# Kernel tuning notes

Hardware: AMD Instinct MI355X
Metric: run time of the kernel (lower is better)

The kernel has to match this reference:

```python
import jax, jax.numpy as jnp
import numpy as np

BETA = 0.1
TRUNC = 1.0
MIN_VALID_RATIO = 0.3


def _wls_affine(x, y, w):
    # Weighted least squares fit of y ~ s*x + t over the last axis.
    sw = w.sum(-1)
    swx = (w * x).sum(-1)
    swy = (w * y).sum(-1)
    swxx = (w * x * x).sum(-1)
    swxy = (w * x * y).sum(-1)
    det = sw * swxx - swx * swx
    det = jnp.where(jnp.abs(det) < 1e-12, 1e-12, det)
    s = (sw * swxy - swx * swy) / det
    t = (swxx * swy - swx * swxy) / det
    return s, t


def _align_depth_affine(x, y, w, trunc):
    # Truncated robust affine alignment: initial WLS fit, then refit with
    # weights of points whose weighted residual exceeds `trunc` zeroed out
    # (falling back to the original weights if everything is truncated).
    s0, t0 = _wls_affine(x, y, w)
    e = w * jnp.abs(s0[..., None] * x + t0[..., None] - y)
    w2 = w * (e < trunc).astype(w.dtype)
    w2 = jnp.where(w2.sum(-1, keepdims=True) > 1e-8, w2, w)
    return _wls_affine(x, y, w2)


def _smooth(err, beta):
    if beta == 0:
        return err
    return jnp.where(err < beta, 0.5 * err * err / beta, err - 0.5 * beta)


def setup_inputs() -> dict:
    key = jax.random.key(0)
    k1, k2, k3 = jax.random.split(key, 3)
    B = 8
    P = 4096  # num_patches
    K = 256   # patch_pixel_count
    N = P * K
    pred_depth = jax.random.uniform(k1, (B, N), jnp.float32, 0.05, 5.0)
    gt_depth = jax.random.uniform(k2, (B, N), jnp.float32, 0.05, 5.0)
    mask = jax.random.bernoulli(k3, 0.8, (B, N))
    global_scale = jnp.ones((B,), jnp.float32)
    return {
        "pred_depth": pred_depth,
        "gt_depth": gt_depth,
        "mask": mask,
        "global_scale": global_scale,
        "num_patches": P,
        "patch_pixel_count": K,
    }


def reference(pred_depth, gt_depth, mask, global_scale, num_patches, patch_pixel_count):
    B = pred_depth.shape[0]
    P, K = num_patches, patch_pixel_count
    x = pred_depth.reshape(B, P, K)
    y = gt_depth.reshape(B, P, K)
    m = mask.reshape(B, P, K).astype(x.dtype)

    valid_ratio = m.mean(-1)                      # (B, P)
    msum = m.sum(-1)
    mean_depth = jnp.where(msum > 0, (y * m).sum(-1) / jnp.maximum(msum, 1.0), 1.0)

    w = m / jnp.maximum(y, 1e-5)                  # alignment weights (B, P, K)
    s, t = _align_depth_affine(x, y, w, TRUNC)    # (B, P) scale / shift per patch

    ratio = s / jnp.maximum(global_scale[:, None], 1e-12)
    gs_ok = jnp.where(global_scale[:, None] > 0, (ratio >= 0.1) & (ratio <= 10.0), True)
    valid = (valid_ratio >= MIN_VALID_RATIO) & (s > 0) & gs_ok  # (B, P)

    aligned = s[..., None] * x + t[..., None]
    pw = m / jnp.maximum(y, 0.1 * mean_depth[..., None])
    patch_loss = _smooth(jnp.abs(aligned - y) * pw, BETA).mean(-1)  # (B, P)

    vf = valid.astype(x.dtype)
    cnt = vf.sum()
    loss = jnp.where(cnt > 0, (patch_loss * vf).sum() / jnp.maximum(cnt, 1.0), 0.0)
    return loss
```

## Files before the change

kernel.cpp:

```cpp
#include <hip/hip_runtime.h>


#define WPB 4
#define PPW 4
#define NSLOTS 64
#define MAXBLK 2048

__device__ __forceinline__ float wredu(float v) {
#define DPP_ADD(ctrl)                                                        \
  v += __int_as_float(__builtin_amdgcn_update_dpp(                           \
      0, __float_as_int(v), (ctrl), 0xf, 0xf, true))
  DPP_ADD(0x111);
  DPP_ADD(0x112);
  DPP_ADD(0x114);
  DPP_ADD(0x118);
  DPP_ADD(0x142);
  DPP_ADD(0x143);
#undef DPP_ADD
  return __int_as_float(__builtin_amdgcn_readlane(__float_as_int(v), 63));
}

__device__ __forceinline__ float rowredu(float v) {
#define DPP_ADD(ctrl)                                                        \
  v += __int_as_float(__builtin_amdgcn_update_dpp(                           \
      0, __float_as_int(v), (ctrl), 0xf, 0xf, true))
  DPP_ADD(0x121);
  DPP_ADD(0x122);
  DPP_ADD(0x124);
  DPP_ADD(0x128);
#undef DPP_ADD
  return v;
}

__device__ __forceinline__ float frcp(float x) {
  return __builtin_amdgcn_rcpf(x);
}

__global__ __launch_bounds__(256) void moge_patch_kernel(
    const float* __restrict__ xg,
    const float* __restrict__ yg,
    const int*   __restrict__ mg,
    const float* __restrict__ gsg,
    const int*   __restrict__ pP,
    const int*   __restrict__ pK,
    int B,
    float* __restrict__ ws) {
  const int P = pP[0];
  const int K = pK[0];
  const int lane = threadIdx.x & 63;
  const int wib  = threadIdx.x >> 6;
  const int total_patches = B * P;
  const float invK = 1.0f / (float)K;

  float wloss = 0.f, wcnt = 0.f;

  if (K == 256) {
    const int row = lane >> 4;
    const int col = lane & 15;
    const int poff = col * 16;
    const int wave_stride = gridDim.x * WPB * PPW;

    for (int pbase = (blockIdx.x * WPB + wib) * PPW; pbase < total_patches;
         pbase += wave_stride) {
      const int patch = pbase + row;
      const bool row_ok = patch < total_patches;
      const long base = (row_ok ? (long)patch * 256L : 0L) + poff;

      float4 xa[4], ya[4]; int4 ma[4];
      #pragma unroll
      for (int j = 0; j < 4; ++j) {
        xa[j] = *(const float4*)(xg + base + 4 * j);
        ya[j] = *(const float4*)(yg + base + 4 * j);
        ma[j] = *(const int4*)(mg + base + 4 * j);
      }
      const float* xr = (const float*)xa;
      const float* yr = (const float*)ya;
      const int*   mi = (const int*)ma;
      float wv[16];

      float sw = 0.f, swx = 0.f, swy = 0.f, swxx = 0.f, swxy = 0.f;
      float msum = 0.f, symsum = 0.f;
      #pragma unroll
      for (int i = 0; i < 16; ++i) {
        const float m = mi[i] ? 1.f : 0.f;
        const float xx = xr[i], yy = yr[i];
        const float w = m * frcp(fmaxf(yy, 1e-5f));
        wv[i] = w;
        const float wx = w * xx;
        sw += w; swx += wx; swy = fmaf(w, yy, swy);
        swxx = fmaf(wx, xx, swxx); swxy = fmaf(wx, yy, swxy);
        msum += m; symsum = fmaf(m, yy, symsum);
      }
      sw = rowredu(sw); swx = rowredu(swx); swy = rowredu(swy);
      swxx = rowredu(swxx); swxy = rowredu(swxy);

      float det = sw * swxx - swx * swx;
      if (fabsf(det) < 1e-12f) det = 1e-12f;
      float rdet = frcp(det);
      const float s0 = (sw * swxy - swx * swy) * rdet;
      const float t0 = (swxx * swy - swx * swxy) * rdet;

      float sw2 = 0.f, swx2 = 0.f, swy2 = 0.f, swxx2 = 0.f, swxy2 = 0.f;
      #pragma unroll
      for (int i = 0; i < 16; ++i) {
        const float xx = xr[i], yy = yr[i], w = wv[i];
        const float e = w * fabsf(fmaf(s0, xx, t0) - yy);
        const float w2 = (e < 1.0f) ? w : 0.f;
        const float w2x = w2 * xx;
        sw2 += w2; swx2 += w2x; swy2 = fmaf(w2, yy, swy2);
        swxx2 = fmaf(w2x, xx, swxx2); swxy2 = fmaf(w2x, yy, swxy2);
      }
      sw2 = rowredu(sw2); swx2 = rowredu(swx2); swy2 = rowredu(swy2);
      swxx2 = rowredu(swxx2); swxy2 = rowredu(swxy2);
      msum = rowredu(msum); symsum = rowredu(symsum);

      if (sw2 > 1e-8f) {
        sw = sw2; swx = swx2; swy = swy2; swxx = swxx2; swxy = swxy2;
      }
      det = sw * swxx - swx * swx;
      if (fabsf(det) < 1e-12f) det = 1e-12f;
      rdet = frcp(det);
      const float s = (sw * swxy - swx * swy) * rdet;
      const float t = (swxx * swy - swx * swxy) * rdet;

      const float mean_depth =
          (msum > 0.f) ? (symsum * frcp(fmaxf(msum, 1.f))) : 1.f;
      const float yfloor = 0.1f * mean_depth;

      float lsum = 0.f;
      #pragma unroll
      for (int i = 0; i < 16; ++i) {
        const float m = (wv[i] > 0.f) ? 1.f : 0.f;
        const float pw = m * frcp(fmaxf(yr[i], yfloor));
        const float err = fabsf(fmaf(s, xr[i], t) - yr[i]) * pw;
        lsum += (err < 0.1f) ? (5.0f * err * err) : (err - 0.05f);
      }
      const float patch_loss = rowredu(lsum) * invK;

      const int pidx = row_ok ? patch : (total_patches - 1);
      const float gs = gsg[(unsigned)pidx / (unsigned)P];
      const float ratio = s * frcp(fmaxf(gs, 1e-12f));
      const bool gs_ok = (gs > 0.f) ? (ratio >= 0.1f && ratio <= 10.0f) : true;
      const bool valid = (msum * invK >= 0.3f) && (s > 0.f) && gs_ok;

      if (col == 0 && row_ok && valid) { wloss += patch_loss; wcnt += 1.f; }
    }
  } else {
    const int wave_stride = gridDim.x * WPB;
    for (int patch = blockIdx.x * WPB + wib; patch < total_patches;
         patch += wave_stride) {
      const long base = (long)patch * (long)K;
      const float* xp = xg + base;
      const float* yp = yg + base;
      const int*   mp = mg + base;

      float sw = 0.f, swx = 0.f, swy = 0.f, swxx = 0.f, swxy = 0.f;
      float msum = 0.f, symsum = 0.f;
      for (int j = lane; j < K; j += 64) {
        const float m = mp[j] ? 1.f : 0.f;
        const float xx = xp[j], yy = yp[j];
        const float w = m * frcp(fmaxf(yy, 1e-5f));
        const float wx = w * xx;
        sw += w; swx += wx; swy = fmaf(w, yy, swy);
        swxx = fmaf(wx, xx, swxx); swxy = fmaf(wx, yy, swxy);
        msum += m; symsum = fmaf(m, yy, symsum);
      }
      sw = wredu(sw); swx = wredu(swx); swy = wredu(swy);
      swxx = wredu(swxx); swxy = wredu(swxy);
      msum = wredu(msum); symsum = wredu(symsum);

      float det = sw * swxx - swx * swx;
      if (fabsf(det) < 1e-12f) det = 1e-12f;
      float rdet = frcp(det);
      const float s0 = (sw * swxy - swx * swy) * rdet;
      const float t0 = (swxx * swy - swx * swxy) * rdet;

      float sw2 = 0.f, swx2 = 0.f, swy2 = 0.f, swxx2 = 0.f, swxy2 = 0.f;
      for (int j = lane; j < K; j += 64) {
        const float m = mp[j] ? 1.f : 0.f;
        const float xx = xp[j], yy = yp[j];
        const float w = m * frcp(fmaxf(yy, 1e-5f));
        const float e = w * fabsf(fmaf(s0, xx, t0) - yy);
        const float w2 = (e < 1.0f) ? w : 0.f;
        const float w2x = w2 * xx;
        sw2 += w2; swx2 += w2x; swy2 = fmaf(w2, yy, swy2);
        swxx2 = fmaf(w2x, xx, swxx2); swxy2 = fmaf(w2x, yy, swxy2);
      }
      sw2 = wredu(sw2); swx2 = wredu(swx2); swy2 = wredu(swy2);
      swxx2 = wredu(swxx2); swxy2 = wredu(swxy2);

      if (sw2 > 1e-8f) {
        sw = sw2; swx = swx2; swy = swy2; swxx = swxx2; swxy = swxy2;
      }
      det = sw * swxx - swx * swx;
      if (fabsf(det) < 1e-12f) det = 1e-12f;
      rdet = frcp(det);
      const float s = (sw * swxy - swx * swy) * rdet;
      const float t = (swxx * swy - swx * swxy) * rdet;

      const float mean_depth =
          (msum > 0.f) ? (symsum * frcp(fmaxf(msum, 1.f))) : 1.f;
      const float yfloor = 0.1f * mean_depth;

      float lsum = 0.f;
      for (int j = lane; j < K; j += 64) {
        const float m = mp[j] ? 1.f : 0.f;
        const float xx = xp[j], yy = yp[j];
        const float pw = m * frcp(fmaxf(yy, yfloor));
        const float err = fabsf(fmaf(s, xx, t) - yy) * pw;
        lsum += (err < 0.1f) ? (5.0f * err * err) : (err - 0.05f);
      }
      const float patch_loss = wredu(lsum) * invK;

      const float gs = gsg[(unsigned)patch / (unsigned)P];
      const float ratio = s * frcp(fmaxf(gs, 1e-12f));
      const bool gs_ok = (gs > 0.f) ? (ratio >= 0.1f && ratio <= 10.0f) : true;
      const bool valid = (msum * invK >= 0.3f) && (s > 0.f) && gs_ok;

      if (lane == 0 && valid) { wloss += patch_loss; wcnt += 1.f; }
    }
  }

  wloss = wredu(wloss);
  wcnt  = wredu(wcnt);
  __shared__ float sl[WPB], sc[WPB];
  if (lane == 0) { sl[wib] = wloss; sc[wib] = wcnt; }
  __syncthreads();
  if (threadIdx.x == 0) {
    float bl = 0.f, bc = 0.f;
    #pragma unroll
    for (int i = 0; i < WPB; ++i) { bl += sl[i]; bc += sc[i]; }
    const int slot = (blockIdx.x & (NSLOTS - 1)) * 32;
    atomicAdd(&ws[slot], bl);
    atomicAdd(&ws[slot + 1], bc);
  }
}

__global__ void finalize_kernel(const float* __restrict__ ws,
                                float* __restrict__ out) {
  const int t = threadIdx.x;
  float l = wredu(ws[t * 32]);
  float c = wredu(ws[t * 32 + 1]);
  if (t == 0) out[0] = (c > 0.f) ? (l / fmaxf(c, 1.f)) : 0.f;
}

extern "C" void kernel_launch(void* const* d_in, const int* in_sizes, int n_in,
                              void* d_out, int out_size, void* d_ws, size_t ws_size,
                              hipStream_t stream) {
  const float* pred = (const float*)d_in[0];
  const float* gt   = (const float*)d_in[1];
  const int*   mask = (const int*)d_in[2];
  const float* gs   = (const float*)d_in[3];
  const int*   pP   = (const int*)d_in[4];
  const int*   pK   = (const int*)d_in[5];
  const int B = in_sizes[3];
  const long total_pixels = (long)in_sizes[0];
  float* ws = (float*)d_ws;

  hipMemsetAsync(ws, 0, NSLOTS * 32 * sizeof(float), stream);

  long est_patches = total_pixels / 256;
  long blocks = (est_patches + WPB * PPW - 1) / (WPB * PPW);
  if (blocks < 1) blocks = 1;
  if (blocks > MAXBLK) blocks = MAXBLK;
  moge_patch_kernel<<<(int)blocks, 256, 0, stream>>>(pred, gt, mask, gs, pP,
                                                     pK, B, ws);
  finalize_kernel<<<1, 64, 0, stream>>>(ws, (float*)d_out);
}
```

Before: 127.9 us.

## Prefetch next patch group in registers, drop memset and atomics for per-block partials

The K=256 loop is restructured to load the next iteration's x, y and mask vectors into registers before computing the current patch group, giving software double buffering that hides global-memory latency. The grid cap is halved so each wave handles more iterations, and per-block partial sums are written directly to distinct workspace slots instead of atomically added into 64 slots. This lets the hipMemsetAsync launch be removed, and a 256-thread finalize kernel reduces all block partials. The cost is doubled register use for the staged tiles, which may lower occupancy, plus one redundant prefetch on the last iteration.

```diff
diff --git a/kernel.cpp b/kernel.cpp
--- a/kernel.cpp
+++ b/kernel.cpp
@@ -3,8 +3,7 @@
 
 #define WPB 4
 #define PPW 4
-#define NSLOTS 64
-#define MAXBLK 2048
+#define MAXBLK 1024
 
 __device__ __forceinline__ float wredu(float v) {
 #define DPP_ADD(ctrl)                                                        \
@@ -60,90 +59,116 @@
     const int poff = col * 16;
     const int wave_stride = gridDim.x * WPB * PPW;
 
-    for (int pbase = (blockIdx.x * WPB + wib) * PPW; pbase < total_patches;
-         pbase += wave_stride) {
-      const int patch = pbase + row;
-      const bool row_ok = patch < total_patches;
-      const long base = (row_ok ? (long)patch * 256L : 0L) + poff;
-
+    int pbase = (blockIdx.x * WPB + wib) * PPW;
+    if (pbase < total_patches) {
       float4 xa[4], ya[4]; int4 ma[4];
-      #pragma unroll
-      for (int j = 0; j < 4; ++j) {
-        xa[j] = *(const float4*)(xg + base + 4 * j);
-        ya[j] = *(const float4*)(yg + base + 4 * j);
-        ma[j] = *(const int4*)(mg + base + 4 * j);
-      }
-      const float* xr = (const float*)xa;
-      const float* yr = (const float*)ya;
-      const int*   mi = (const int*)ma;
-      float wv[16];
-
-      float sw = 0.f, swx = 0.f, swy = 0.f, swxx = 0.f, swxy = 0.f;
-      float msum = 0.f, symsum = 0.f;
-      #pragma unroll
-      for (int i = 0; i < 16; ++i) {
-        const float m = mi[i] ? 1.f : 0.f;
-        const float xx = xr[i], yy = yr[i];
-        const float w = m * frcp(fmaxf(yy, 1e-5f));
-        wv[i] = w;
-        const float wx = w * xx;
-        sw += w; swx += wx; swy = fmaf(w, yy, swy);
-        swxx = fmaf(wx, xx, swxx); swxy = fmaf(wx, yy, swxy);
-        msum += m; symsum = fmaf(m, yy, symsum);
-      }
-      sw = rowredu(sw); swx = rowredu(swx); swy = rowredu(swy);
-      swxx = rowredu(swxx); swxy = rowredu(swxy);
-
-      float det = sw * swxx - swx * swx;
-      if (fabsf(det) < 1e-12f) det = 1e-12f;
-      float rdet = frcp(det);
-      const float s0 = (sw * swxy - swx * swy) * rdet;
-      const float t0 = (swxx * swy - swx * swxy) * rdet;
-
-      float sw2 = 0.f, swx2 = 0.f, swy2 = 0.f, swxx2 = 0.f, swxy2 = 0.f;
-      #pragma unroll
-      for (int i = 0; i < 16; ++i) {
-        const float xx = xr[i], yy = yr[i], w = wv[i];
-        const float e = w * fabsf(fmaf(s0, xx, t0) - yy);
-        const float w2 = (e < 1.0f) ? w : 0.f;
-        const float w2x = w2 * xx;
-        sw2 += w2; swx2 += w2x; swy2 = fmaf(w2, yy, swy2);
-        swxx2 = fmaf(w2x, xx, swxx2); swxy2 = fmaf(w2x, yy, swxy2);
-      }
-      sw2 = rowredu(sw2); swx2 = rowredu(swx2); swy2 = rowredu(swy2);
-      swxx2 = rowredu(swxx2); swxy2 = rowredu(swxy2);
-      msum = rowredu(msum); symsum = rowredu(symsum);
-
-      if (sw2 > 1e-8f) {
-        sw = sw2; swx = swx2; swy = swy2; swxx = swxx2; swxy = swxy2;
-      }
-      det = sw * swxx - swx * swx;
-      if (fabsf(det) < 1e-12f) det = 1e-12f;
-      rdet = frcp(det);
-      const float s = (sw * swxy - swx * swy) * rdet;
-      const float t = (swxx * swy - swx * swxy) * rdet;
-
-      const float mean_depth =
-          (msum > 0.f) ? (symsum * frcp(fmaxf(msum, 1.f))) : 1.f;
-      const float yfloor = 0.1f * mean_depth;
-
-      float lsum = 0.f;
-      #pragma unroll
-      for (int i = 0; i < 16; ++i) {
-        const float m = (wv[i] > 0.f) ? 1.f : 0.f;
-        const float pw = m * frcp(fmaxf(yr[i], yfloor));
-        const float err = fabsf(fmaf(s, xr[i], t) - yr[i]) * pw;
-        lsum += (err < 0.1f) ? (5.0f * err * err) : (err - 0.05f);
-      }
-      const float patch_loss = rowredu(lsum) * invK;
-
-      const int pidx = row_ok ? patch : (total_patches - 1);
-      const float gs = gsg[(unsigned)pidx / (unsigned)P];
-      const float ratio = s * frcp(fmaxf(gs, 1e-12f));
-      const bool gs_ok = (gs > 0.f) ? (ratio >= 0.1f && ratio <= 10.0f) : true;
-      const bool valid = (msum * invK >= 0.3f) && (s > 0.f) && gs_ok;
-
-      if (col == 0 && row_ok && valid) { wloss += patch_loss; wcnt += 1.f; }
+      {
+        const int patch0 = pbase + row;
+        const long base =
+            ((patch0 < total_patches) ? (long)patch0 * 256L : 0L) + poff;
+        #pragma unroll
+        for (int j = 0; j < 4; ++j) {
+          xa[j] = *(const float4*)(xg + base + 4 * j);
+          ya[j] = *(const float4*)(yg + base + 4 * j);
+          ma[j] = *(const int4*)(mg + base + 4 * j);
+        }
+      }
+
+      for (;;) {
+        const int nbase_p = pbase + wave_stride;
+        const bool has_next = nbase_p < total_patches;
+        float4 nxa[4], nya[4]; int4 nma[4];
+        {
+          const int np = nbase_p + row;
+          const long nb =
+              ((has_next && np < total_patches) ? (long)np * 256L : 0L) + poff;
+          #pragma unroll
+          for (int j = 0; j < 4; ++j) {
+            nxa[j] = *(const float4*)(xg + nb + 4 * j);
+            nya[j] = *(const float4*)(yg + nb + 4 * j);
+            nma[j] = *(const int4*)(mg + nb + 4 * j);
+          }
+        }
+
+        const int patch = pbase + row;
+        const bool row_ok = patch < total_patches;
+        const float* xr = (const float*)xa;
+        const float* yr = (const float*)ya;
+        const int*   mi = (const int*)ma;
+        float wv[16];
+
+        float sw = 0.f, swx = 0.f, swy = 0.f, swxx = 0.f, swxy = 0.f;
+        float msum = 0.f, symsum = 0.f;
+        #pragma unroll
+        for (int i = 0; i < 16; ++i) {
+          const float m = mi[i] ? 1.f : 0.f;
+          const float xx = xr[i], yy = yr[i];
+          const float w = m * frcp(fmaxf(yy, 1e-5f));
+          wv[i] = w;
+          const float wx = w * xx;
+          sw += w; swx += wx; swy = fmaf(w, yy, swy);
+          swxx = fmaf(wx, xx, swxx); swxy = fmaf(wx, yy, swxy);
+          msum += m; symsum = fmaf(m, yy, symsum);
+        }
+        sw = rowredu(sw); swx = rowredu(swx); swy = rowredu(swy);
+        swxx = rowredu(swxx); swxy = rowredu(swxy);
+
+        float det = sw * swxx - swx * swx;
+        if (fabsf(det) < 1e-12f) det = 1e-12f;
+        float rdet = frcp(det);
+        const float s0 = (sw * swxy - swx * swy) * rdet;
+        const float t0 = (swxx * swy - swx * swxy) * rdet;
+
+        float sw2 = 0.f, swx2 = 0.f, swy2 = 0.f, swxx2 = 0.f, swxy2 = 0.f;
+        #pragma unroll
+        for (int i = 0; i < 16; ++i) {
+          const float xx = xr[i], yy = yr[i], w = wv[i];
+          const float e = w * fabsf(fmaf(s0, xx, t0) - yy);
+          const float w2 = (e < 1.0f) ? w : 0.f;
+          const float w2x = w2 * xx;
+          sw2 += w2; swx2 += w2x; swy2 = fmaf(w2, yy, swy2);
+          swxx2 = fmaf(w2x, xx, swxx2); swxy2 = fmaf(w2x, yy, swxy2);
+        }
+        sw2 = rowredu(sw2); swx2 = rowredu(swx2); swy2 = rowredu(swy2);
+        swxx2 = rowredu(swxx2); swxy2 = rowredu(swxy2);
+        msum = rowredu(msum); symsum = rowredu(symsum);
+
+        if (sw2 > 1e-8f) {
+          sw = sw2; swx = swx2; swy = swy2; swxx = swxx2; swxy = swxy2;
+        }
+        det = sw * swxx - swx * swx;
+        if (fabsf(det) < 1e-12f) det = 1e-12f;
+        rdet = frcp(det);
+        const float s = (sw * swxy - swx * swy) * rdet;
+        const float t = (swxx * swy - swx * swxy) * rdet;
+
+        const float mean_depth =
+            (msum > 0.f) ? (symsum * frcp(fmaxf(msum, 1.f))) : 1.f;
+        const float yfloor = 0.1f * mean_depth;
+
+        float lsum = 0.f;
+        #pragma unroll
+        for (int i = 0; i < 16; ++i) {
+          const float m = (wv[i] > 0.f) ? 1.f : 0.f;
+          const float pw = m * frcp(fmaxf(yr[i], yfloor));
+          const float err = fabsf(fmaf(s, xr[i], t) - yr[i]) * pw;
+          lsum += (err < 0.1f) ? (5.0f * err * err) : (err - 0.05f);
+        }
+        const float patch_loss = rowredu(lsum) * invK;
+
+        const int pidx = row_ok ? patch : (total_patches - 1);
+        const float gs = gsg[(unsigned)pidx / (unsigned)P];
+        const float ratio = s * frcp(fmaxf(gs, 1e-12f));
+        const bool gs_ok = (gs > 0.f) ? (ratio >= 0.1f && ratio <= 10.0f) : true;
+        const bool valid = (msum * invK >= 0.3f) && (s > 0.f) && gs_ok;
+
+        if (col == 0 && row_ok && valid) { wloss += patch_loss; wcnt += 1.f; }
+
+        if (!has_next) break;
+        pbase = nbase_p;
+        #pragma unroll
+        for (int j = 0; j < 4; ++j) { xa[j] = nxa[j]; ya[j] = nya[j]; ma[j] = nma[j]; }
+      }
     }
   } else {
     const int wave_stride = gridDim.x * WPB;
@@ -230,18 +255,29 @@
     float bl = 0.f, bc = 0.f;
     #pragma unroll
     for (int i = 0; i < WPB; ++i) { bl += sl[i]; bc += sc[i]; }
-    const int slot = (blockIdx.x & (NSLOTS - 1)) * 32;
-    atomicAdd(&ws[slot], bl);
-    atomicAdd(&ws[slot + 1], bc);
+    ws[blockIdx.x * 32]     = bl;
+    ws[blockIdx.x * 32 + 1] = bc;
   }
 }
 
-__global__ void finalize_kernel(const float* __restrict__ ws,
-                                float* __restrict__ out) {
-  const int t = threadIdx.x;
-  float l = wredu(ws[t * 32]);
-  float c = wredu(ws[t * 32 + 1]);
-  if (t == 0) out[0] = (c > 0.f) ? (l / fmaxf(c, 1.f)) : 0.f;
+__global__ __launch_bounds__(256) void finalize_kernel(
+    const float* __restrict__ ws, float* __restrict__ out, int nblocks) {
+  const int lane = threadIdx.x & 63;
+  const int wib  = threadIdx.x >> 6;
+  float l = 0.f, c = 0.f;
+  for (int i = threadIdx.x; i < nblocks; i += 256) {
+    l += ws[i * 32];
+    c += ws[i * 32 + 1];
+  }
+  l = wredu(l); c = wredu(c);
+  __shared__ float sl[4], sc[4];
+  if (lane == 0) { sl[wib] = l; sc[wib] = c; }
+  __syncthreads();
+  if (threadIdx.x == 0) {
+    const float L = sl[0] + sl[1] + sl[2] + sl[3];
+    const float C = sc[0] + sc[1] + sc[2] + sc[3];
+    out[0] = (C > 0.f) ? (L / fmaxf(C, 1.f)) : 0.f;
+  }
 }
 
 extern "C" void kernel_launch(void* const* d_in, const int* in_sizes, int n_in,
@@ -257,13 +293,11 @@
   const long total_pixels = (long)in_sizes[0];
   float* ws = (float*)d_ws;
 
-  hipMemsetAsync(ws, 0, NSLOTS * 32 * sizeof(float), stream);
-
   long est_patches = total_pixels / 256;
   long blocks = (est_patches + WPB * PPW - 1) / (WPB * PPW);
   if (blocks < 1) blocks = 1;
   if (blocks > MAXBLK) blocks = MAXBLK;
   moge_patch_kernel<<<(int)blocks, 256, 0, stream>>>(pred, gt, mask, gs, pP,
                                                      pK, B, ws);
-  finalize_kernel<<<1, 64, 0, stream>>>(ws, (float*)d_out);
-}
+  finalize_kernel<<<1, 256, 0, stream>>>(ws, (float*)d_out, (int)blocks);
+}
```

Result: no change. 128.5 us (+0.4%).
